# Performance work log

Hardware: AMD Instinct MI355X
Metric: run time of the kernel (lower is better)

Reference implementation:

```python
import jax, jax.numpy as jnp
import numpy as np

EMBED_DIM = 1024
NUM_HEADS = 16
HEAD_DIM = EMBED_DIM // NUM_HEADS
B, S = 2, 2048
NEG = -1e20


def setup_inputs() -> dict:
    key = jax.random.key(0)
    ks = jax.random.split(key, 8)
    scale = 0.02
    return {
        "query": jax.random.normal(ks[0], (B, S, EMBED_DIM), jnp.float32),
        "keys": jax.random.normal(ks[1], (B, S, EMBED_DIM), jnp.float32),
        "values": jax.random.normal(ks[2], (B, S, EMBED_DIM), jnp.float32),
        "mask": jax.random.randint(ks[3], (1, 1, S, S), 0, 2, jnp.int32),
        "Wq": jax.random.normal(ks[4], (EMBED_DIM, EMBED_DIM), jnp.float32) * scale,
        "Wk": jax.random.normal(ks[5], (EMBED_DIM, EMBED_DIM), jnp.float32) * scale,
        "Wv": jax.random.normal(ks[6], (EMBED_DIM, EMBED_DIM), jnp.float32) * scale,
        "Wo": jax.random.normal(ks[7], (EMBED_DIM, EMBED_DIM), jnp.float32) * scale,
        "bo": jnp.zeros((EMBED_DIM,), jnp.float32),
    }


def reference(query, keys, values, mask, Wq, Wk, Wv, Wo, bo):
    N, Lq, _ = query.shape
    Lk = keys.shape[1]
    # torch nn.Linear: y = x @ W.T  (bias=False for Q/K/V)
    Q = (query @ Wq.T).reshape(N, Lq, NUM_HEADS, HEAD_DIM)
    K = (keys @ Wk.T).reshape(N, Lk, NUM_HEADS, HEAD_DIM)
    V = (values @ Wv.T).reshape(N, Lk, NUM_HEADS, HEAD_DIM)
    # NOTE: source scales by sqrt(embed_dim), not sqrt(head_dim) — kept faithful.
    energy = jnp.einsum("nqhd,nkhd->nhqk", Q, K) / jnp.sqrt(
        jnp.asarray(EMBED_DIM, Q.dtype)
    )
    energy = jnp.where(mask == 0, jnp.asarray(NEG, energy.dtype), energy)
    attention = jax.nn.softmax(energy, axis=3)
    out = jnp.einsum("nhqk,nkhd->nqhd", attention, V).reshape(N, Lq, EMBED_DIM)
    return out @ Wo.T + bo
```

## Files before the change

### kernel.cpp

```cpp
#include <hip/hip_runtime.h>
#include <stdint.h>

typedef __bf16 bf16;
typedef __bf16 bf16x4 __attribute__((ext_vector_type(4)));
typedef __bf16 bf16x8 __attribute__((ext_vector_type(8)));
typedef float f32x4 __attribute__((ext_vector_type(4)));
typedef float f32x16 __attribute__((ext_vector_type(16)));
typedef unsigned int uintx2 __attribute__((ext_vector_type(2)));
typedef unsigned int uintx4 __attribute__((ext_vector_type(4)));

#define MFMA16(a, b, c) __builtin_amdgcn_mfma_f32_16x16x32_bf16((a), (b), (c), 0, 0, 0)
#define MFMA32(a, b, c) __builtin_amdgcn_mfma_f32_32x32x16_bf16((a), (b), (c), 0, 0, 0)

__device__ __forceinline__ void gload16(const bf16* g, bf16* l) {
    __builtin_amdgcn_global_load_lds(
        (const __attribute__((address_space(1))) void*)g,
        (__attribute__((address_space(3))) void*)l, 16, 0, 0);
}

__device__ __forceinline__ float fast_exp2(float x) {
#if __has_builtin(__builtin_amdgcn_exp2f)
    return __builtin_amdgcn_exp2f(x);
#else
    return exp2f(x);
#endif
}

__global__ __launch_bounds__(256) void cvt_kernel(
    const float* __restrict__ q, const float* __restrict__ k, const float* __restrict__ v,
    const float* __restrict__ wq, const float* __restrict__ wk,
    const float* __restrict__ wv, const float* __restrict__ wo,
    const int* __restrict__ mask,
    bf16* __restrict__ qb, bf16* __restrict__ kb, bf16* __restrict__ vb,
    bf16* __restrict__ wqb, bf16* __restrict__ wkb, bf16* __restrict__ wvb,
    bf16* __restrict__ wob, unsigned long long* __restrict__ maskb)
{
    int z = blockIdx.z;
    if (z == 7) {
#pragma unroll
        for (int it = 0; it < 8; ++it) {
            int gid  = it * 524288 + blockIdx.x * 256 + threadIdx.x;
            int lane = gid & 63;
            int mv = mask[gid];
            unsigned long long bits = __ballot(mv != 0);
            if (lane == 0) maskb[gid >> 6] = bits;
        }
        return;
    }
    const float* src; bf16* dst; int n;
    switch (z) {
        case 0:  src = q;  dst = qb;  n = 4194304; break;
        case 1:  src = k;  dst = kb;  n = 4194304; break;
        case 2:  src = v;  dst = vb;  n = 4194304; break;
        case 3:  src = wq; dst = wqb; n = 1048576; break;
        case 4:  src = wk; dst = wkb; n = 1048576; break;
        case 5:  src = wv; dst = wvb; n = 1048576; break;
        default: src = wo; dst = wob; n = 1048576; break;
    }
    int i = (blockIdx.x * 256 + threadIdx.x) * 8;
    if (i >= n) return;
    float4 f0 = *(const float4*)(src + i);
    float4 f1 = *(const float4*)(src + i + 4);
    bf16x8 o;
    o[0] = (bf16)f0.x; o[1] = (bf16)f0.y; o[2] = (bf16)f0.z; o[3] = (bf16)f0.w;
    o[4] = (bf16)f1.x; o[5] = (bf16)f1.y; o[6] = (bf16)f1.z; o[7] = (bf16)f1.w;
    *(bf16x8*)(dst + i) = o;
}

template <int OUTMODE>
__global__ __launch_bounds__(256) void gemm_kernel(
    const bf16* __restrict__ A0, const bf16* __restrict__ A1, const bf16* __restrict__ A2,
    const bf16* __restrict__ B0, const bf16* __restrict__ B1, const bf16* __restrict__ B2,
    bf16* __restrict__ C0, bf16* __restrict__ C1, bf16* __restrict__ Vt,
    const float* __restrict__ bias, float* __restrict__ outf)
{
    constexpr int SMEM = (OUTMODE == 0) ? (128 * 136) : 16384;
    __shared__ bf16 smem[SMEM];
    bf16* At0 = smem;
    bf16* At1 = smem + 4096;
    bf16* Bt0 = smem + 8192;
    bf16* Bt1 = smem + 12288;

    const int f = blockIdx.x + 8 * blockIdx.y + ((OUTMODE == 0) ? 256 * blockIdx.z : 0);
    const int xcd = f & 7, sidx = f >> 3;
    const int z  = sidx >> 5;
    const int m0 = (xcd * 4 + (sidx & 3)) * 128;
    const int n0 = ((sidx >> 2) & 7) * 128;

    const bf16* A = (z == 0) ? A0 : (z == 1) ? A1 : A2;
    const bf16* B = (z == 0) ? B0 : (z == 1) ? B1 : B2;

    const int tid  = threadIdx.x;
    const int lane = tid & 63;
    const int wave = tid >> 6;
    const int quad = lane >> 4;
    const int l16  = lane & 15;
    const int wm = (wave >> 1) * 64;
    const int wn = (wave & 1) * 64;

    const int lrow = lane >> 2;
    const int lcol = (lane & 3) * 8;

    f32x4 acc[4][4] = {};

    const bf16* Ag = A + (size_t)(m0 + lrow) * 1024 + lcol;
    const bf16* Bg = B + (size_t)(n0 + lrow) * 1024 + lcol;

    auto stage = [&](bf16* Atb, bf16* Btb, int k0) {
#pragma unroll
        for (int j = 0; j < 2; ++j)
            gload16(Ag + (size_t)(wave * 32 + j * 16) * 1024 + k0,
                    Atb + (wave * 32 + j * 16) * 32);
#pragma unroll
        for (int j = 0; j < 2; ++j)
            gload16(Bg + (size_t)(wave * 32 + j * 16) * 1024 + k0,
                    Btb + (wave * 32 + j * 16) * 32);
    };

    auto body = [&](const bf16* Ac, const bf16* Bc, bf16* An, bf16* Bn, int k0) {
        __syncthreads();
        if (k0 + 32 < 1024) stage(An, Bn, k0 + 32);

        bf16x8 af[4], bg[4];
#pragma unroll
        for (int i = 0; i < 4; ++i)
            af[i] = *(const bf16x8*)(Ac + (wm + i * 16 + l16) * 32 + quad * 8);
#pragma unroll
        for (int j = 0; j < 4; ++j)
            bg[j] = *(const bf16x8*)(Bc + (wn + j * 16 + l16) * 32 + quad * 8);
#pragma unroll
        for (int i = 0; i < 4; ++i)
#pragma unroll
            for (int j = 0; j < 4; ++j)
                acc[i][j] = MFMA16(af[i], bg[j], acc[i][j]);
    };

    stage(At0, Bt0, 0);
    for (int k0 = 0; k0 < 1024; k0 += 64) {
        body(At0, Bt0, At1, Bt1, k0);
        body(At1, Bt1, At0, Bt0, k0 + 32);
    }

    if constexpr (OUTMODE == 0) {
        if (z == 2) {
            __syncthreads();
            const int qsw = ((quad & 1) << 1) | (quad >> 1);
#pragma unroll
            for (int i = 0; i < 4; ++i)
#pragma unroll
                for (int j = 0; j < 4; ++j) {
                    int e  = wn + j * 16 + l16;
                    int sp = wm + i * 16 + qsw * 4;
                    bf16x4 v4;
#pragma unroll
                    for (int r = 0; r < 4; ++r) v4[r] = (bf16)acc[i][j][r];
                    *(bf16x4*)(smem + e * 136 + sp) = v4;
                }
            __syncthreads();
            const int bq = m0 >> 11;
            const int srow = m0 & 2047;
#pragma unroll
            for (int c = 0; c < 2; ++c) {
                int idx = c * 256 + tid;
                int e = idx >> 2, sc = (idx & 3) * 32;
                bf16* dst = Vt + (size_t)(bq * 1024 + n0 + e) * 2048 + srow + sc;
#pragma unroll
                for (int kk = 0; kk < 4; ++kk)
                    *(bf16x8*)(dst + kk * 8) =
                        *(const bf16x8*)(smem + e * 136 + sc + kk * 8);
            }
            return;
        }
        bf16* C = (z == 0) ? C0 : C1;
        const float cs = (z == 0) ? 0.0450842200277800f : 1.0f;
#pragma unroll
        for (int i = 0; i < 4; ++i)
#pragma unroll
            for (int j = 0; j < 4; ++j) {
                int row = m0 + wm + i * 16 + quad * 4;
                int col = n0 + wn + j * 16 + l16;
#pragma unroll
                for (int r = 0; r < 4; ++r)
                    C[(row + r) * 1024 + col] = (bf16)(acc[i][j][r] * cs);
            }
    } else {
#pragma unroll
        for (int j = 0; j < 4; ++j) {
            int col = n0 + wn + j * 16 + l16;
            float bj = bias[col];
#pragma unroll
            for (int i = 0; i < 4; ++i) {
                int row = m0 + wm + i * 16 + quad * 4;
#pragma unroll
                for (int r = 0; r < 4; ++r)
                    outf[(row + r) * 1024 + col] = acc[i][j][r] + bj;
            }
        }
    }
}

__global__ __launch_bounds__(512, 4) void flash_kernel(
    const bf16* __restrict__ Q, const bf16* __restrict__ K, const bf16* __restrict__ Vt,
    const unsigned long long* __restrict__ maskb, bf16* __restrict__ O)
{
    __shared__ char smem[65536];

    const int tid  = threadIdx.x;
    const int lane = tid & 63;
    const int wave = tid >> 6;
    const int half = wave >> 2;
    const int w4   = wave & 3;
    const int l32  = lane & 31;
    const int hl   = lane >> 5;
    const int l7   = lane & 7;

    const int flat = blockIdx.x + 16 * (blockIdx.y + 16 * blockIdx.z);
    const int xcd  = flat & 7;
    const int slot = flat >> 3;
    const int bh   = xcd * 4 + (slot >> 4);
    const int h  = bh & 15;
    const int b  = bh >> 4;
    const int q0 = (slot & 15) * 128;
    const int qt = q0 + w4 * 32;

    bf16* hbase = (bf16*)smem + half * 16384;
    bf16* K0 = hbase;
    bf16* K1 = hbase + 4096;
    bf16* V0 = hbase + 8192;
    bf16* V1 = hbase + 12288;

    const bf16* Qb = Q + (size_t)(b * 2048 + qt + l32) * 1024 + h * 64 + hl * 8;
    bf16x8 qf[4];
#pragma unroll
    for (int ks = 0; ks < 4; ++ks) qf[ks] = *(const bf16x8*)(Qb + ks * 16);

    bf16x8 ones;
#pragma unroll
    for (int j = 0; j < 8; ++j) ones[j] = (bf16)1.0f;

    f32x16 acc[2] = {};
    f32x16 lacc = {};

    const int dmarow = lane >> 3;
    const int dmacol = (l7 ^ dmarow) * 8;
    const bf16* Kg = K + (size_t)(b * 2048 + w4 * 16 + dmarow) * 1024 + h * 64 + dmacol;
    const bf16* Vg = Vt + (size_t)((b * 16 + h) * 64 + w4 * 16 + dmarow) * 2048 + dmacol;
    const unsigned long long* Mg = maskb + (size_t)(qt + l32) * 32 + half * 16;
    const int kbase = half * 1024;

    auto stage = [&](bf16* Kd, bf16* Vd, int ktAbs) {
        gload16(Kg + (size_t)ktAbs * 1024,       Kd + (w4 * 16) * 64);
        gload16(Kg + (size_t)(ktAbs + 8) * 1024, Kd + (w4 * 16 + 8) * 64);
        gload16(Vg + ktAbs,                      Vd + (w4 * 16) * 64);
        gload16(Vg + ktAbs + 8 * 2048,           Vd + (w4 * 16 + 8) * 64);
    };

    unsigned long long mw = Mg[0];
    stage(K0, V0, kbase);

    auto body = [&](const bf16* Kc, const bf16* Vc, bf16* Kn, bf16* Vn, int it) {
        __syncthreads();
        unsigned long long mw_next = 0;
        if (it + 1 < 16) {
            stage(Kn, Vn, kbase + (it + 1) * 64);
            mw_next = Mg[it + 1];
        }

        bf16x8 pa[4];
#pragma unroll
        for (int t = 0; t < 2; ++t) {
            f32x16 s = {};
            __builtin_amdgcn_s_setprio(1);
#pragma unroll
            for (int ks = 0; ks < 4; ++ks) {
                bf16x8 ka = *(const bf16x8*)(Kc + (t * 32 + l32) * 64 +
                                             (((ks * 2 + hl) ^ l7) * 8));
                s = MFMA32(ka, qf[ks], s);
            }
            __builtin_amdgcn_s_setprio(0);
            unsigned mwt = (unsigned)(mw >> (t * 32 + 4 * hl));
            unsigned W[4][2];
#pragma unroll
            for (int g = 0; g < 4; ++g) {
                bf16x4 pv;
#pragma unroll
                for (int r = 0; r < 4; ++r) {
                    float ev = fast_exp2(s[g * 4 + r]);
                    unsigned msk = (unsigned)((int)(mwt << (31 - (8 * g + r))) >> 31);
                    unsigned evu = __builtin_bit_cast(unsigned, ev) & msk;
                    pv[r] = (bf16)__builtin_bit_cast(float, evu);
                }
                uintx2 u = __builtin_bit_cast(uintx2, pv);
                W[g][0] = u[0];
                W[g][1] = u[1];
            }
#pragma unroll
            for (int kh = 0; kh < 2; ++kh) {
                uintx4 aw = { W[2 * kh][0], W[2 * kh][1],
                              W[2 * kh + 1][0], W[2 * kh + 1][1] };
                pa[t * 2 + kh] = __builtin_bit_cast(bf16x8, aw);
            }
        }

        __builtin_amdgcn_s_setprio(1);
#pragma unroll
        for (int dt = 0; dt < 2; ++dt)
#pragma unroll
            for (int ks = 0; ks < 4; ++ks) {
                bf16x8 vb = *(const bf16x8*)(Vc + (dt * 32 + l32) * 64 +
                                             (((ks * 2 + hl) ^ l7) * 8));
                acc[dt] = MFMA32(pa[ks], vb, acc[dt]);
            }
#pragma unroll
        for (int ks = 0; ks < 4; ++ks)
            lacc = MFMA32(pa[ks], ones, lacc);
        __builtin_amdgcn_s_setprio(0);

        mw = mw_next;
    };

    for (int it = 0; it < 16; it += 2) {
        body(K0, V0, K1, V1, it);
        body(K1, V1, K0, V0, it + 1);
    }

    __syncthreads();
    float* cb = (float*)smem;
    float* ex = cb + (w4 * 64 + lane) * 4;
    if (half == 1) {
#pragma unroll
        for (int i = 0; i < 4; ++i) {
            f32x4 t0, t1, t2;
#pragma unroll
            for (int j = 0; j < 4; ++j) {
                t0[j] = acc[0][i * 4 + j];
                t1[j] = acc[1][i * 4 + j];
                t2[j] = lacc[i * 4 + j];
            }
            *(f32x4*)(ex + (i + 0) * 1024) = t0;
            *(f32x4*)(ex + (i + 4) * 1024) = t1;
            *(f32x4*)(ex + (i + 8) * 1024) = t2;
        }
    }
    __syncthreads();
    if (half == 0) {
#pragma unroll
        for (int i = 0; i < 4; ++i) {
            f32x4 t0 = *(const f32x4*)(ex + (i + 0) * 1024);
            f32x4 t1 = *(const f32x4*)(ex + (i + 4) * 1024);
            f32x4 t2 = *(const f32x4*)(ex + (i + 8) * 1024);
#pragma unroll
            for (int j = 0; j < 4; ++j) {
                acc[0][i * 4 + j] += t0[j];
                acc[1][i * 4 + j] += t1[j];
                lacc[i * 4 + j]   += t2[j];
            }
        }

        const size_t obase = (size_t)(b * 2048 + qt) * 1024 + h * 64;
#pragma unroll
        for (int g = 0; g < 4; ++g)
#pragma unroll
            for (int r = 0; r < 4; ++r) {
                int qr = 4 * hl + 8 * g + r;
                float inv = 1.0f / lacc[g * 4 + r];
                O[obase + (size_t)qr * 1024 + l32]      = (bf16)(acc[0][g * 4 + r] * inv);
                O[obase + (size_t)qr * 1024 + 32 + l32] = (bf16)(acc[1][g * 4 + r] * inv);
            }
    }
}

extern "C" void kernel_launch(void* const* d_in, const int* in_sizes, int n_in,
                              void* d_out, int out_size, void* d_ws, size_t ws_size,
                              hipStream_t stream)
{
    const float* q  = (const float*)d_in[0];
    const float* k  = (const float*)d_in[1];
    const float* v  = (const float*)d_in[2];
    const int* mask = (const int*)d_in[3];
    const float* wq = (const float*)d_in[4];
    const float* wk = (const float*)d_in[5];
    const float* wv = (const float*)d_in[6];
    const float* wo = (const float*)d_in[7];
    const float* bo = (const float*)d_in[8];
    float* out = (float*)d_out;

    char* p = (char*)d_ws;
    auto alloc = [&](size_t bytes) {
        char* r = p;
        p += (bytes + 255) & ~(size_t)255;
        return r;
    };
    const size_t SB = (size_t)4096 * 1024 * 2;
    const size_t WB = (size_t)1024 * 1024 * 2;
    bf16* qb  = (bf16*)alloc(SB);
    bf16* kb  = (bf16*)alloc(SB);
    bf16* vb  = (bf16*)alloc(SB);
    bf16* wqb = (bf16*)alloc(WB);
    bf16* wkb = (bf16*)alloc(WB);
    bf16* wvb = (bf16*)alloc(WB);
    bf16* wob = (bf16*)alloc(WB);
    bf16* Qp  = (bf16*)alloc(SB);
    bf16* Kp  = (bf16*)alloc(SB);
    bf16* Vtp = (bf16*)alloc(SB);
    bf16* Ob  = (bf16*)alloc(SB);
    unsigned long long* maskb = (unsigned long long*)alloc(2048 * 32 * 8);

    cvt_kernel<<<dim3(2048, 1, 8), 256, 0, stream>>>(
        q, k, v, wq, wk, wv, wo, mask, qb, kb, vb, wqb, wkb, wvb, wob, maskb);

    gemm_kernel<0><<<dim3(8, 32, 3), 256, 0, stream>>>(
        qb, kb, vb, wqb, wkb, wvb, Qp, Kp, Vtp, nullptr, nullptr);

    flash_kernel<<<dim3(16, 16, 2), 512, 0, stream>>>(Qp, Kp, Vtp, maskb, Ob);

    gemm_kernel<1><<<dim3(8, 32, 1), 256, 0, stream>>>(
        Ob, nullptr, nullptr, wob, nullptr, nullptr,
        nullptr, nullptr, nullptr, bo, out);
}
```

Measured before the change: 233.7 us.

## Triple-buffer GEMM loads, narrow output-projection tiles, vectorize mask packing

The GEMM main loop moves from a double-buffered __syncthreads loop to a three-stage LDS ring. It prefetches two k-steps ahead and uses explicit vmcnt waits plus a raw barrier, so global loads overlap more MFMA work. The output-projection GEMM switches to 128x64 tiles with twice as many blocks to fill more CUs. Mask packing now reads int4 vectors and combines bits with shuffles instead of one ballot per element. The costs are more LDS per block and hand-tuned vmcnt counts that must match the number of loads issued per stage.

```diff
diff --git a/kernel.cpp b/kernel.cpp
--- a/kernel.cpp
+++ b/kernel.cpp
@@ -37,14 +37,22 @@
 {
     int z = blockIdx.z;
     if (z == 7) {
-#pragma unroll
-        for (int it = 0; it < 8; ++it) {
-            int gid  = it * 524288 + blockIdx.x * 256 + threadIdx.x;
-            int lane = gid & 63;
-            int mv = mask[gid];
-            unsigned long long bits = __ballot(mv != 0);
-            if (lane == 0) maskb[gid >> 6] = bits;
-        }
+        int t16 = blockIdx.x * 256 + threadIdx.x;
+        if (t16 >= 262144) return;
+        const int4* mp = (const int4*)mask + (size_t)t16 * 4;
+        unsigned bits = 0;
+#pragma unroll
+        for (int c = 0; c < 4; ++c) {
+            int4 a = mp[c];
+            bits |= (unsigned)(a.x != 0) << (c * 4 + 0);
+            bits |= (unsigned)(a.y != 0) << (c * 4 + 1);
+            bits |= (unsigned)(a.z != 0) << (c * 4 + 2);
+            bits |= (unsigned)(a.w != 0) << (c * 4 + 3);
+        }
+        unsigned long long u = (unsigned long long)bits << (16 * (threadIdx.x & 3));
+        u |= __shfl_xor(u, 1, 64);
+        u |= __shfl_xor(u, 2, 64);
+        if ((threadIdx.x & 3) == 0) maskb[t16 >> 2] = u;
         return;
     }
     const float* src; bf16* dst; int n;
@@ -74,18 +82,16 @@
     bf16* __restrict__ C0, bf16* __restrict__ C1, bf16* __restrict__ Vt,
     const float* __restrict__ bias, float* __restrict__ outf)
 {
-    constexpr int SMEM = (OUTMODE == 0) ? (128 * 136) : 16384;
-    __shared__ bf16 smem[SMEM];
-    bf16* At0 = smem;
-    bf16* At1 = smem + 4096;
-    bf16* Bt0 = smem + 8192;
-    bf16* Bt1 = smem + 12288;
+    constexpr int TN    = (OUTMODE == 0) ? 128 : 64;
+    constexpr int NI    = TN / 32;
+    constexpr int BUFSZ = 4096 + TN * 32;
+    __shared__ bf16 smem[3 * BUFSZ];
 
     const int f = blockIdx.x + 8 * blockIdx.y + ((OUTMODE == 0) ? 256 * blockIdx.z : 0);
     const int xcd = f & 7, sidx = f >> 3;
-    const int z  = sidx >> 5;
+    const int z  = (OUTMODE == 0) ? (sidx >> 5) : 0;
     const int m0 = (xcd * 4 + (sidx & 3)) * 128;
-    const int n0 = ((sidx >> 2) & 7) * 128;
+    const int n0 = (OUTMODE == 0) ? ((sidx >> 2) & 7) * 128 : (sidx >> 2) * 64;
 
     const bf16* A = (z == 0) ? A0 : (z == 1) ? A1 : A2;
     const bf16* B = (z == 0) ? B0 : (z == 1) ? B1 : B2;
@@ -96,50 +102,72 @@
     const int quad = lane >> 4;
     const int l16  = lane & 15;
     const int wm = (wave >> 1) * 64;
-    const int wn = (wave & 1) * 64;
+    const int wn = (wave & 1) * (TN / 2);
 
     const int lrow = lane >> 2;
     const int lcol = (lane & 3) * 8;
 
-    f32x4 acc[4][4] = {};
+    f32x4 acc[4][NI] = {};
 
     const bf16* Ag = A + (size_t)(m0 + lrow) * 1024 + lcol;
     const bf16* Bg = B + (size_t)(n0 + lrow) * 1024 + lcol;
 
-    auto stage = [&](bf16* Atb, bf16* Btb, int k0) {
+    bf16* buf0 = smem;
+    bf16* buf1 = smem + BUFSZ;
+    bf16* buf2 = smem + 2 * BUFSZ;
+
+    auto stage = [&](bf16* base, int k0) {
 #pragma unroll
         for (int j = 0; j < 2; ++j)
             gload16(Ag + (size_t)(wave * 32 + j * 16) * 1024 + k0,
-                    Atb + (wave * 32 + j * 16) * 32);
-#pragma unroll
-        for (int j = 0; j < 2; ++j)
-            gload16(Bg + (size_t)(wave * 32 + j * 16) * 1024 + k0,
-                    Btb + (wave * 32 + j * 16) * 32);
+                    base + (wave * 32 + j * 16) * 32);
+        bf16* Btb = base + 4096;
+        if constexpr (OUTMODE == 0) {
+#pragma unroll
+            for (int j = 0; j < 2; ++j)
+                gload16(Bg + (size_t)(wave * 32 + j * 16) * 1024 + k0,
+                        Btb + (wave * 32 + j * 16) * 32);
+        } else {
+            gload16(Bg + (size_t)(wave * 16) * 1024 + k0, Btb + (wave * 16) * 32);
+        }
     };
 
-    auto body = [&](const bf16* Ac, const bf16* Bc, bf16* An, bf16* Bn, int k0) {
-        __syncthreads();
-        if (k0 + 32 < 1024) stage(An, Bn, k0 + 32);
-
-        bf16x8 af[4], bg[4];
+    auto step = [&](bf16* cb, bf16* sb, int k0) {
+        if (k0 == 992) {
+            asm volatile("s_waitcnt vmcnt(0)" ::: "memory");
+        } else if constexpr (OUTMODE == 0) {
+            asm volatile("s_waitcnt vmcnt(4)" ::: "memory");
+        } else {
+            asm volatile("s_waitcnt vmcnt(3)" ::: "memory");
+        }
+        __builtin_amdgcn_s_barrier();
+        __builtin_amdgcn_sched_barrier(0);
+        if (k0 + 64 < 1024) stage(sb, k0 + 64);
+
+        const bf16* Btb = cb + 4096;
+        bf16x8 af[4], bg[NI];
 #pragma unroll
         for (int i = 0; i < 4; ++i)
-            af[i] = *(const bf16x8*)(Ac + (wm + i * 16 + l16) * 32 + quad * 8);
-#pragma unroll
-        for (int j = 0; j < 4; ++j)
-            bg[j] = *(const bf16x8*)(Bc + (wn + j * 16 + l16) * 32 + quad * 8);
+            af[i] = *(const bf16x8*)(cb + (wm + i * 16 + l16) * 32 + quad * 8);
+#pragma unroll
+        for (int j = 0; j < NI; ++j)
+            bg[j] = *(const bf16x8*)(Btb + (wn + j * 16 + l16) * 32 + quad * 8);
 #pragma unroll
         for (int i = 0; i < 4; ++i)
 #pragma unroll
-            for (int j = 0; j < 4; ++j)
+            for (int j = 0; j < NI; ++j)
                 acc[i][j] = MFMA16(af[i], bg[j], acc[i][j]);
     };
 
-    stage(At0, Bt0, 0);
-    for (int k0 = 0; k0 < 1024; k0 += 64) {
-        body(At0, Bt0, At1, Bt1, k0);
-        body(At1, Bt1, At0, Bt0, k0 + 32);
-    }
+    stage(buf0, 0);
+    stage(buf1, 32);
+    for (int k0 = 0; k0 < 960; k0 += 96) {
+        step(buf0, buf2, k0);
+        step(buf1, buf0, k0 + 32);
+        step(buf2, buf1, k0 + 64);
+    }
+    step(buf0, buf2, 960);
+    step(buf1, buf0, 992);
 
     if constexpr (OUTMODE == 0) {
         if (z == 2) {
@@ -185,7 +213,7 @@
             }
     } else {
 #pragma unroll
-        for (int j = 0; j < 4; ++j) {
+        for (int j = 0; j < NI; ++j) {
             int col = n0 + wn + j * 16 + l16;
             float bj = bias[col];
 #pragma unroll
@@ -414,7 +442,7 @@
 
     flash_kernel<<<dim3(16, 16, 2), 512, 0, stream>>>(Qp, Kp, Vtp, maskb, Ob);
 
-    gemm_kernel<1><<<dim3(8, 32, 1), 256, 0, stream>>>(
+    gemm_kernel<1><<<dim3(8, 64, 1), 256, 0, stream>>>(
         Ob, nullptr, nullptr, wob, nullptr, nullptr,
         nullptr, nullptr, nullptr, bo, out);
 }
```

Measured after the change: 227.9 us. 1.03x faster.
